# Kernel optimization log

Hardware: AMD Instinct MI355X
Metric: run time of the kernel (lower is better)

Reference implementation:

```python
import math
import jax, jax.numpy as jnp
import numpy as np

B, T, C = 4, 2048, 1024
H = 16
HS = C // H  # head_size = 64

def setup_inputs() -> dict:
    key = jax.random.key(0)
    k1, k2, k3 = jax.random.split(key, 3)
    x = jax.random.normal(k1, (B, T, C), dtype=jnp.float32)
    W_qkv = jax.random.normal(k2, (C, 3 * C), dtype=jnp.float32) * (1.0 / math.sqrt(C))
    W_proj = jax.random.normal(k3, (C, C), dtype=jnp.float32) * (1.0 / math.sqrt(C))
    b_proj = jnp.zeros((C,), dtype=jnp.float32)
    return {"x": x, "W_qkv": W_qkv, "W_proj": W_proj, "b_proj": b_proj}

def reference(x, W_qkv, W_proj, b_proj):
    Bx, Tx, Cx = x.shape
    qkv = x @ W_qkv  # [B,T,3C]
    q, k, v = jnp.split(qkv, 3, axis=-1)
    # [B,T,C] -> [B,H,T,HS]
    def heads(t):
        return t.reshape(Bx, Tx, H, HS).transpose(0, 2, 1, 3)
    q, k, v = heads(q), heads(k), heads(v)
    scores = jnp.einsum('bhqd,bhkd->bhqk', q, k) / math.sqrt(HS)
    causal = jnp.tril(jnp.ones((Tx, Tx), dtype=bool))
    scores = jnp.where(causal, scores, -jnp.inf)
    attn = jax.nn.softmax(scores, axis=-1)
    out = jnp.einsum('bhqk,bhkd->bhqd', attn, v)  # [B,H,T,HS]
    out = out.transpose(0, 2, 1, 3).reshape(Bx, Tx, Cx)
    return out @ W_proj + b_proj
```

## Files before the change

### kernel.cpp

```cpp
#include <hip/hip_runtime.h>
#include <hip/hip_bf16.h>
#include <cstdint>
#include <cstddef>

using bf16 = __hip_bfloat16;
typedef __attribute__((ext_vector_type(8))) short short8;
typedef __attribute__((ext_vector_type(4))) float floatx4;

#define B_ 4
#define T_ 2048
#define C_ 1024
#define H_ 16
#define HS_ 64
#define BT_ (B_*T_)
#define N3C (3*C_)

#define MFMA16(a,b,c) __builtin_amdgcn_mfma_f32_16x16x32_bf16((a),(b),(c),0,0,0)

#if __has_builtin(__builtin_amdgcn_exp2f)
#define EXP2(x) __builtin_amdgcn_exp2f(x)
#else
#define EXP2(x) exp2f(x)
#endif

static __device__ __forceinline__ void gld16(const bf16* g, bf16* l) {
  __builtin_amdgcn_global_load_lds(
      (const __attribute__((address_space(1))) unsigned int*)g,
      (__attribute__((address_space(3))) unsigned int*)l, 16, 0, 0);
}

__global__ void k_cast(const float* __restrict__ in, bf16* __restrict__ out, int n4) {
  int i = blockIdx.x * blockDim.x + threadIdx.x;
  if (i >= n4) return;
  float4 v = ((const float4*)in)[i];
  union { bf16 b[4]; uint2 u; } cvt;
  cvt.b[0] = __float2bfloat16(v.x);
  cvt.b[1] = __float2bfloat16(v.y);
  cvt.b[2] = __float2bfloat16(v.z);
  cvt.b[3] = __float2bfloat16(v.w);
  ((uint2*)out)[i] = cvt.u;
}

__global__ void k_tcast(const float* __restrict__ in, bf16* __restrict__ out, int K, int N) {
  __shared__ float tile[64][65];
  const int k0 = blockIdx.y * 64, n0 = blockIdx.x * 64;
  const int tid = threadIdx.x;
  const int r = tid >> 6, c = tid & 63;
  #pragma unroll
  for (int j = 0; j < 16; ++j)
    tile[r + j*4][c] = in[(size_t)(k0 + r + j*4) * N + n0 + c];
  __syncthreads();
  #pragma unroll
  for (int j = 0; j < 16; ++j) {
    int rr = r + j*4;
    out[(size_t)(n0 + rr) * K + k0 + c] = __float2bfloat16(tile[c][rr]);
  }
}

__global__ void k_vtrans(const bf16* __restrict__ Vb, bf16* __restrict__ Vt) {
  __shared__ unsigned short tile[64*65];
  const int tid = threadIdx.x;
  const int bh = blockIdx.y, t0 = blockIdx.x * 64;
  const unsigned int* src = (const unsigned int*)(Vb + (size_t)bh * T_ * HS_ + (size_t)t0 * HS_);
  #pragma unroll
  for (int it = 0; it < 8; ++it) {
    int id = it*256 + tid;
    int row = id >> 5, cd = id & 31;
    unsigned int v = src[row*32 + cd];
    tile[row*65 + cd*2]     = (unsigned short)(v & 0xffff);
    tile[row*65 + cd*2 + 1] = (unsigned short)(v >> 16);
  }
  __syncthreads();
  bf16* dst = Vt + (size_t)bh * HS_ * T_ + t0;
  #pragma unroll
  for (int it = 0; it < 8; ++it) {
    int o = it*256 + tid;
    int d = o >> 5, tp = o & 31;
    int k0p = tp + (tp & 16);
    unsigned int lo = tile[k0p*65 + d];
    unsigned int hi = tile[(k0p + 16)*65 + d];
    ((unsigned int*)(dst + (size_t)d * T_))[tp] = lo | (hi << 16);
  }
}

template<int MODE>
__global__ __launch_bounds__(256, 2)
void k_gemm(const bf16* __restrict__ A, const bf16* __restrict__ Bt,
            int N, int K,
            bf16* __restrict__ Qb, bf16* __restrict__ Kb, bf16* __restrict__ Vb,
            float* __restrict__ Out, const float* __restrict__ bias)
{
  __shared__ bf16 sA[128*32];
  __shared__ bf16 sB[128*32];
  const int tid  = threadIdx.x;
  const int lane = tid & 63, wave = tid >> 6;
  const int quad = lane >> 4, l16 = lane & 15;
  const int wm = wave >> 1, wn = wave & 1;
  const int m0 = blockIdx.y * 128, n0 = blockIdx.x * 128;

  const int ra = tid >> 2;
  const int ka = (tid & 3) * 8;
  const bf16* aptr = A  + (size_t)(m0 + ra) * K + ka;
  const bf16* bptr = Bt + (size_t)(n0 + ra) * K + ka;
  bf16* sa0 = &sA[tid*8]; bf16* sa1 = &sA[2048 + tid*8];
  bf16* sb0 = &sB[tid*8]; bf16* sb1 = &sB[2048 + tid*8];
  const size_t rowjump = (size_t)64 * K;

  floatx4 acc[4][4] = {};

  for (int k0 = 0; k0 < K; k0 += 32) {
    __syncthreads();
    gld16(aptr + k0,           sa0);
    gld16(aptr + rowjump + k0, sa1);
    gld16(bptr + k0,           sb0);
    gld16(bptr + rowjump + k0, sb1);
    __syncthreads();
    short8 af[4], bfm[4];
    #pragma unroll
    for (int i = 0; i < 4; ++i)
      af[i] = *(const short8*)&sA[(wm*64 + i*16 + l16) * 32 + quad*8];
    #pragma unroll
    for (int i = 0; i < 4; ++i)
      bfm[i] = *(const short8*)&sB[(wn*64 + i*16 + l16) * 32 + quad*8];
    #pragma unroll
    for (int i = 0; i < 4; ++i)
      #pragma unroll
      for (int j = 0; j < 4; ++j)
        acc[i][j] = MFMA16(af[i], bfm[j], acc[i][j]);
  }

  #pragma unroll
  for (int i = 0; i < 4; ++i) {
    const int rowb = m0 + wm*64 + i*16 + quad*4;
    #pragma unroll
    for (int j = 0; j < 4; ++j) {
      const int col = n0 + wn*64 + j*16 + l16;
      #pragma unroll
      for (int r = 0; r < 4; ++r) {
        const float v = acc[i][j][r];
        const int rr = rowb + r;
        if (MODE == 0) {
          const int b = rr >> 11, t = rr & 2047;
          const int h = (col >> 6) & 15, d = col & 63;
          const size_t addr = (((size_t)(b*H_ + h) * T_ + t) << 6) + d;
          if (col < C_) {
            Qb[addr] = __float2bfloat16(v * 0.18033688f);
          } else if (col < 2*C_) {
            Kb[addr] = __float2bfloat16(v);
          } else {
            Vb[addr] = __float2bfloat16(v);
          }
        } else {
          Out[(size_t)rr * N + col] = v + bias[col];
        }
      }
    }
  }
}

__global__ __launch_bounds__(256, 2)
void k_attn(const bf16* __restrict__ Q, const bf16* __restrict__ K,
            const bf16* __restrict__ Vt, bf16* __restrict__ att)
{
  __shared__ bf16 kbuf[2][64*64];
  __shared__ bf16 vbuf[2][64*64];
  __shared__ bf16 pbuf[4][32*64];

  const int tid  = threadIdx.x;
  const int lane = tid & 63, wave = tid >> 6;
  const int quad = lane >> 4, l16 = lane & 15;
  const int x7 = l16 & 7;

  const int g  = blockIdx.x;
  const int bh = (g & 7) * 8 + (g >> 6);
  const int bx = (g >> 3) & 7;
  const int b = bh >> 4, h = bh & 15;

  const bf16* Qp = Q  + (size_t)bh * T_ * HS_;
  const bf16* Kp = K  + (size_t)bh * T_ * HS_;
  const bf16* Vp = Vt + (size_t)bh * HS_ * T_;

  const int qbase[2] = { (15-bx)*128 + wave*32, bx*128 + wave*32 };
  const int ntk0 = 32 - 2*bx;
  const int ntk1 = 2*bx + 2;

  short8 qf[2][2][2];
  #pragma unroll
  for (int t = 0; t < 2; ++t)
    #pragma unroll
    for (int mt = 0; mt < 2; ++mt)
      #pragma unroll
      for (int ss = 0; ss < 2; ++ss)
        qf[t][mt][ss] = *(const short8*)(Qp + (size_t)(qbase[t] + mt*16 + l16) * HS_ + ss*32 + quad*8);

  floatx4 o[2][2][4] = {};
  float lrow[2][2][4] = {};

  const bf16* kg[2]; const bf16* vg[2];
  int ldsoff[2];
  #pragma unroll
  for (int it = 0; it < 2; ++it) {
    const int c = it*256 + tid;
    const int row = c >> 3;
    const int col = (c & 7) ^ (row & 7);
    kg[it] = Kp + (size_t)row * HS_ + col*8;
    vg[it] = Vp + (size_t)row * T_ + col*8;
    ldsoff[it] = c*8;
  }

  bf16* pw = pbuf[wave];
  unsigned int* pw32 = (unsigned int*)pw;
  const int c0 = l16 >> 2;
  const int dwl = l16 & 3;

  for (int i = 0; i <= ntk0; ++i) {
    __syncthreads();
    if (i < ntk0) {
      const int stk0 = i * 64;
      bf16* kb = kbuf[i & 1];
      bf16* vb = vbuf[i & 1];
      #pragma unroll
      for (int it = 0; it < 2; ++it) {
        gld16(kg[it] + (size_t)stk0 * HS_, kb + ldsoff[it]);
        gld16(vg[it] + stk0,               vb + ldsoff[it]);
      }
    }
    if (i == 0) continue;
    const int tk  = i - 1;
    const int tk0 = tk * 64;
    const bf16* kb = kbuf[tk & 1];
    const bf16* vb = vbuf[tk & 1];

    #pragma unroll
    for (int t = 0; t < 2; ++t) {
      if (t == 1 && tk >= ntk1) break;
      if (tk0 > qbase[t] + 31) continue;

      floatx4 s[2][4] = {};
      #pragma unroll
      for (int nt = 0; nt < 4; ++nt) {
        const int key = nt*16 + l16;
        #pragma unroll
        for (int ss = 0; ss < 2; ++ss) {
          short8 kf = *(const short8*)&kb[(key*8 + ((ss*4+quad) ^ x7))*8];
          s[0][nt] = MFMA16(qf[t][0][ss], kf, s[0][nt]);
          s[1][nt] = MFMA16(qf[t][1][ss], kf, s[1][nt]);
        }
      }

      if (tk0 + 63 > qbase[t]) {
        #pragma unroll
        for (int mt = 0; mt < 2; ++mt)
          #pragma unroll
          for (int nt = 0; nt < 4; ++nt) {
            const int key = tk0 + nt*16 + l16;
            #pragma unroll
            for (int r = 0; r < 4; ++r) {
              const int qr = qbase[t] + mt*16 + quad*4 + r;
              if (key > qr) s[mt][nt][r] = -1e30f;
            }
          }
      }

      #pragma unroll
      for (int mt = 0; mt < 2; ++mt) {
        #pragma unroll
        for (int r = 0; r < 4; ++r) {
          const float p0 = EXP2(s[mt][0][r]), p1 = EXP2(s[mt][1][r]);
          const float p2 = EXP2(s[mt][2][r]), p3 = EXP2(s[mt][3][r]);
          lrow[t][mt][r] += (p0 + p1) + (p2 + p3);
          const int q = mt*16 + quad*4 + r;
          const unsigned w0 = __builtin_amdgcn_perm(__float_as_uint(p1), __float_as_uint(p0), 0x07060302u);
          const unsigned w1 = __builtin_amdgcn_perm(__float_as_uint(p3), __float_as_uint(p2), 0x07060302u);
          pw32[q*32 + (((c0 + q)     & 7) << 2) + dwl] = w0;
          pw32[q*32 + (((c0 + q + 4) & 7) << 2) + dwl] = w1;
        }
      }

      #pragma unroll
      for (int ss = 0; ss < 2; ++ss) {
        short8 pf0 = *(const short8*)&pw[l16*64      + ((4*ss + quad + l16) & 7)*8];
        short8 pf1 = *(const short8*)&pw[(16+l16)*64 + ((4*ss + quad + l16) & 7)*8];
        #pragma unroll
        for (int nd = 0; nd < 4; ++nd) {
          const int d = nd*16 + l16;
          short8 vf = *(const short8*)&vb[(d*8 + ((ss*4+quad) ^ x7))*8];
          o[t][0][nd] = MFMA16(pf0, vf, o[t][0][nd]);
          o[t][1][nd] = MFMA16(pf1, vf, o[t][1][nd]);
        }
      }
    }
  }

  #pragma unroll
  for (int t = 0; t < 2; ++t) {
    #pragma unroll
    for (int mt = 0; mt < 2; ++mt) {
      #pragma unroll
      for (int r = 0; r < 4; ++r) {
        float lsum = lrow[t][mt][r];
        lsum += __shfl_xor(lsum, 1);
        lsum += __shfl_xor(lsum, 2);
        lsum += __shfl_xor(lsum, 4);
        lsum += __shfl_xor(lsum, 8);
        const float inv = 1.0f / lsum;
        const int tt = qbase[t] + mt*16 + quad*4 + r;
        #pragma unroll
        for (int nd = 0; nd < 4; ++nd)
          att[(size_t)(b*T_ + tt) * C_ + h*64 + nd*16 + l16] =
              __float2bfloat16(o[t][mt][nd][r] * inv);
      }
    }
  }
}

extern "C" void kernel_launch(void* const* d_in, const int* in_sizes, int n_in,
                              void* d_out, int out_size, void* d_ws, size_t ws_size,
                              hipStream_t stream) {
  const float* x     = (const float*)d_in[0];
  const float* Wqkv  = (const float*)d_in[1];
  const float* Wproj = (const float*)d_in[2];
  const float* bproj = (const float*)d_in[3];
  float* out = (float*)d_out;

  char* ws = (char*)d_ws;
  bf16* xb     = (bf16*)(ws + 0);
  bf16* wqkvT  = (bf16*)(ws + 16777216);
  bf16* wprojT = (bf16*)(ws + 23068672);
  bf16* Qb     = (bf16*)(ws + 25165824);
  bf16* Kb     = (bf16*)(ws + 41943040);
  bf16* Vt     = (bf16*)(ws + 58720256);
  bf16* att    = (bf16*)(ws + 75497472);
  bf16* Vb     = att;

  k_cast<<<dim3(BT_*C_/4/256), 256, 0, stream>>>(x, xb, BT_*C_/4);
  k_tcast<<<dim3(N3C/64, C_/64), 256, 0, stream>>>(Wqkv, wqkvT, C_, N3C);
  k_tcast<<<dim3(C_/64, C_/64), 256, 0, stream>>>(Wproj, wprojT, C_, C_);
  k_gemm<0><<<dim3(N3C/128, BT_/128), 256, 0, stream>>>(
      xb, wqkvT, N3C, C_, Qb, Kb, Vb, nullptr, nullptr);
  k_vtrans<<<dim3(T_/64, B_*H_), 256, 0, stream>>>(Vb, Vt);
  k_attn<<<dim3(512), 256, 0, stream>>>(Qb, Kb, Vt, att);
  k_gemm<1><<<dim3(C_/128, BT_/128), 256, 0, stream>>>(
      att, wprojT, C_, C_, nullptr, nullptr, nullptr, out, bproj);
}
```

Before: 257.6 us.

## Double-buffer GEMM LDS tiles, swizzle LDS layout, remap blocks per XCD

The GEMM kernel now double-buffers its shared-memory A/B tiles so the global-to-LDS loads for the next K step overlap the MFMA work on the current one, with one barrier per iteration. It also XOR-swizzles the 16-byte chunk columns on both the load and fragment-read sides to cut LDS bank conflicts. Blocks are launched on a 1D grid and remapped so that row blocks are spread by XCD index, aiming for better L2 reuse of A rows within each XCD. This doubles LDS use per block, which may reduce occupancy relative to the two-blocks-per-CU launch bound.

```diff
diff --git a/kernel.cpp b/kernel.cpp
--- a/kernel.cpp
+++ b/kernel.cpp
@@ -83,50 +83,62 @@
   }
 }
 
-template<int MODE>
+template<int MODE, int NB>
 __global__ __launch_bounds__(256, 2)
 void k_gemm(const bf16* __restrict__ A, const bf16* __restrict__ Bt,
             int N, int K,
             bf16* __restrict__ Qb, bf16* __restrict__ Kb, bf16* __restrict__ Vb,
             float* __restrict__ Out, const float* __restrict__ bias)
 {
-  __shared__ bf16 sA[128*32];
-  __shared__ bf16 sB[128*32];
+  __shared__ bf16 sA[2][128*32];
+  __shared__ bf16 sB[2][128*32];
   const int tid  = threadIdx.x;
   const int lane = tid & 63, wave = tid >> 6;
   const int quad = lane >> 4, l16 = lane & 15;
   const int wm = wave >> 1, wn = wave & 1;
-  const int m0 = blockIdx.y * 128, n0 = blockIdx.x * 128;
+
+  const int g = blockIdx.x;
+  const int xcd = g & 7;
+  const int local = g >> 3;
+  const int nb = local % NB;
+  const int mb = (local / NB) * 8 + xcd;
+  const int m0 = mb * 128, n0 = nb * 128;
 
   const int ra = tid >> 2;
-  const int ka = (tid & 3) * 8;
-  const bf16* aptr = A  + (size_t)(m0 + ra) * K + ka;
-  const bf16* bptr = Bt + (size_t)(n0 + ra) * K + ka;
-  bf16* sa0 = &sA[tid*8]; bf16* sa1 = &sA[2048 + tid*8];
-  bf16* sb0 = &sB[tid*8]; bf16* sb1 = &sB[2048 + tid*8];
+  const int gc = (tid & 3) ^ ((ra >> 1) & 3);
+  const bf16* aptr = A  + (size_t)(m0 + ra) * K + gc*8;
+  const bf16* bptr = Bt + (size_t)(n0 + ra) * K + gc*8;
   const size_t rowjump = (size_t)64 * K;
 
   floatx4 acc[4][4] = {};
-
-  for (int k0 = 0; k0 < K; k0 += 32) {
+  const int KI = K >> 5;
+  const int pc = quad ^ ((l16 >> 1) & 3);
+
+  for (int i = 0; i <= KI; ++i) {
     __syncthreads();
-    gld16(aptr + k0,           sa0);
-    gld16(aptr + rowjump + k0, sa1);
-    gld16(bptr + k0,           sb0);
-    gld16(bptr + rowjump + k0, sb1);
-    __syncthreads();
+    if (i < KI) {
+      const int k0 = i << 5;
+      bf16* sa = sA[i & 1]; bf16* sb = sB[i & 1];
+      gld16(aptr + k0,           sa + tid*8);
+      gld16(aptr + rowjump + k0, sa + 2048 + tid*8);
+      gld16(bptr + k0,           sb + tid*8);
+      gld16(bptr + rowjump + k0, sb + 2048 + tid*8);
+    }
+    if (i == 0) continue;
+    const bf16* sa = sA[(i-1) & 1];
+    const bf16* sb = sB[(i-1) & 1];
     short8 af[4], bfm[4];
     #pragma unroll
-    for (int i = 0; i < 4; ++i)
-      af[i] = *(const short8*)&sA[(wm*64 + i*16 + l16) * 32 + quad*8];
-    #pragma unroll
-    for (int i = 0; i < 4; ++i)
-      bfm[i] = *(const short8*)&sB[(wn*64 + i*16 + l16) * 32 + quad*8];
-    #pragma unroll
-    for (int i = 0; i < 4; ++i)
+    for (int ii = 0; ii < 4; ++ii)
+      af[ii] = *(const short8*)&sa[(wm*64 + ii*16 + l16) * 32 + pc*8];
+    #pragma unroll
+    for (int ii = 0; ii < 4; ++ii)
+      bfm[ii] = *(const short8*)&sb[(wn*64 + ii*16 + l16) * 32 + pc*8];
+    #pragma unroll
+    for (int ii = 0; ii < 4; ++ii)
       #pragma unroll
       for (int j = 0; j < 4; ++j)
-        acc[i][j] = MFMA16(af[i], bfm[j], acc[i][j]);
+        acc[ii][j] = MFMA16(af[ii], bfm[j], acc[ii][j]);
   }
 
   #pragma unroll
@@ -336,10 +348,10 @@
   k_cast<<<dim3(BT_*C_/4/256), 256, 0, stream>>>(x, xb, BT_*C_/4);
   k_tcast<<<dim3(N3C/64, C_/64), 256, 0, stream>>>(Wqkv, wqkvT, C_, N3C);
   k_tcast<<<dim3(C_/64, C_/64), 256, 0, stream>>>(Wproj, wprojT, C_, C_);
-  k_gemm<0><<<dim3(N3C/128, BT_/128), 256, 0, stream>>>(
+  k_gemm<0, 24><<<dim3(1536), 256, 0, stream>>>(
       xb, wqkvT, N3C, C_, Qb, Kb, Vb, nullptr, nullptr);
   k_vtrans<<<dim3(T_/64, B_*H_), 256, 0, stream>>>(Vb, Vt);
   k_attn<<<dim3(512), 256, 0, stream>>>(Qb, Kb, Vt, att);
-  k_gemm<1><<<dim3(C_/128, BT_/128), 256, 0, stream>>>(
+  k_gemm<1, 8><<<dim3(512), 256, 0, stream>>>(
       att, wprojT, C_, C_, nullptr, nullptr, nullptr, out, bproj);
 }
```

Result: no change. 253.9 us (-1.4%).
